# Optimization experiments

Hardware: AMD Instinct MI355X
Metric: run time of the kernel (lower is better)

Reference implementation:

```python
import jax, jax.numpy as jnp
import numpy as np

B, D, H, K = 32768, 784, 500, 50


def setup_inputs() -> dict:
    key = jax.random.key(0)
    ks = jax.random.split(key, 12)
    s = 0.02  # weight init scale
    return {
        "x": jax.random.uniform(ks[0], (B, D), dtype=jnp.float32),
        "u": jax.random.uniform(ks[1], (B, K), dtype=jnp.float32),
        "enc_w1": jax.random.normal(ks[2], (D, H), dtype=jnp.float32) * s,
        "enc_b1": jnp.zeros((H,), jnp.float32),
        "w_alpha": jax.random.normal(ks[3], (H, K), dtype=jnp.float32) * s,
        "b_alpha": jnp.zeros((K,), jnp.float32),
        "w_beta": jax.random.normal(ks[4], (H, K), dtype=jnp.float32) * s,
        "b_beta": jnp.zeros((K,), jnp.float32),
        "dec_w1": jax.random.normal(ks[5], (K, H), dtype=jnp.float32) * s,
        "dec_b1": jnp.zeros((H,), jnp.float32),
        "dec_w2": jax.random.normal(ks[6], (H, D), dtype=jnp.float32) * s,
        "dec_b2": jnp.zeros((D,), jnp.float32),
    }


def reference(x, u, enc_w1, enc_b1, w_alpha, b_alpha, w_beta, b_beta,
              dec_w1, dec_b1, dec_w2, dec_b2):
    # encode
    h = jax.nn.relu(x @ enc_w1 + enc_b1)                       # [B,H]
    alpha = jax.nn.softplus(h @ w_alpha + b_alpha)             # [B,K] > 0
    beta = jax.nn.softplus(h @ w_beta + b_beta)                # [B,K] > 0
    # Kumaraswamy inverse-CDF sample: v = (1 - u^(1/beta))^(1/alpha)
    v = (1.0 - u ** (1.0 / beta)) ** (1.0 / alpha)             # [B,K]
    # stick-breaking: pi[k] = v[k] * prod_{j<k}(1 - v[j])  (exclusive cumprod)
    cp = jnp.cumprod(1.0 - v, axis=-1)                         # [B,K]
    pi = v * jnp.concatenate([jnp.ones_like(v[:, :1]), cp[:, :-1]], axis=-1)
    # decode
    hd = jax.nn.relu(pi @ dec_w1 + dec_b1)                     # [B,H]
    recon_x = jax.nn.sigmoid(hd @ dec_w2 + dec_b2)             # [B,D]
    return recon_x, alpha, beta
```

## Files before the change

### kernel.cpp

```cpp
#include <hip/hip_runtime.h>
#include <math.h>


typedef __bf16 bf16x8 __attribute__((ext_vector_type(8)));
typedef float f32x4 __attribute__((ext_vector_type(4)));

#define BATCH 32768
#define BM 128
#define BN 128
#define BK 64

__device__ __forceinline__ unsigned short bf16_bits(float f) {
    __bf16 b = (__bf16)f;
    return __builtin_bit_cast(unsigned short, b);
}

__device__ __forceinline__ void gll16(const unsigned short* src, unsigned short* ldsdst) {
    __builtin_amdgcn_global_load_lds(
        (const __attribute__((address_space(1))) unsigned int*)src,
        (__attribute__((address_space(3))) unsigned int*)ldsdst,
        16, 0, 0);
}

template<int MODE, bool AF32>
__global__ __launch_bounds__(256) void mfma_gemm(
    const void* __restrict__ Av,
    const unsigned short* __restrict__ Bt,
    const float* __restrict__ bias,
    void* __restrict__ Cv,
    int Kpad, int Kreal, int lda, int ldc, int Nreal, int nbx)
{
    __shared__ unsigned short As[BM * BK];
    __shared__ unsigned short Bs[BN * BK];

    const int nwg = gridDim.x;
    const int orig = blockIdx.x;
    const int q = nwg >> 3, r8 = nwg & 7;
    const int xcd = orig & 7;
    const int chunkbase = (xcd < r8) ? xcd * (q + 1) : r8 * (q + 1) + (xcd - r8) * q;
    const int wgid = chunkbase + (orig >> 3);
    const int bn = wgid % nbx;
    const size_t block_m = (size_t)(wgid / nbx) * BM;
    const int block_n = bn * BN;

    const int tid = threadIdx.x;
    const int l = tid & 63;
    const int wid = tid >> 6;
    const int wr = wid >> 1, wc = wid & 1;

    const int lr = l & 15;
    const int kh = l >> 4;

    f32x4 acc[4][4] = {};

    for (int k0 = 0; k0 < Kpad; k0 += BK) {
        #pragma unroll
        for (int i = 0; i < 4; ++i) {
            int chunk = wid * 4 + i;
            int gid = chunk * 64 + l;
            int r = gid >> 3;
            int kgs = (gid & 7) ^ (r & 7);
            gll16(Bt + (size_t)(block_n + r) * Kpad + k0 + kgs * 8, Bs + chunk * 512);
        }
        if (AF32) {
            const float* Af = (const float*)Av;
            #pragma unroll
            for (int i = 0; i < 4; ++i) {
                int gid = i * 256 + tid;
                int r = gid >> 3, kg = gid & 7;
                int gk = k0 + kg * 8;
                union { __bf16 b[8]; uint4 u4; } pk;
                if (gk < Kreal) {
                    const float4* p = (const float4*)(Af + (block_m + r) * (size_t)lda + gk);
                    float4 f0 = p[0], f1 = p[1];
                    pk.b[0] = (__bf16)f0.x; pk.b[1] = (__bf16)f0.y;
                    pk.b[2] = (__bf16)f0.z; pk.b[3] = (__bf16)f0.w;
                    pk.b[4] = (__bf16)f1.x; pk.b[5] = (__bf16)f1.y;
                    pk.b[6] = (__bf16)f1.z; pk.b[7] = (__bf16)f1.w;
                } else {
                    pk.u4 = make_uint4(0, 0, 0, 0);
                }
                *(uint4*)(As + r * 64 + ((kg ^ (r & 7)) * 8)) = pk.u4;
            }
        } else {
            const unsigned short* Ab = (const unsigned short*)Av;
            #pragma unroll
            for (int i = 0; i < 4; ++i) {
                int chunk = wid * 4 + i;
                int gid = chunk * 64 + l;
                int r = gid >> 3;
                int kgs = (gid & 7) ^ (r & 7);
                gll16(Ab + (block_m + r) * (size_t)lda + k0 + kgs * 8, As + chunk * 512);
            }
        }
        __syncthreads();

        #pragma unroll
        for (int s = 0; s < 2; ++s) {
            bf16x8 af[4], bf[4];
            #pragma unroll
            for (int mi = 0; mi < 4; ++mi) {
                int row = wr * 64 + mi * 16 + lr;
                int g = (s * 4 + kh) ^ (row & 7);
                af[mi] = *(const bf16x8*)(As + row * 64 + g * 8);
            }
            #pragma unroll
            for (int ni = 0; ni < 4; ++ni) {
                int row = wc * 64 + ni * 16 + lr;
                int g = (s * 4 + kh) ^ (row & 7);
                bf[ni] = *(const bf16x8*)(Bs + row * 64 + g * 8);
            }
            #pragma unroll
            for (int mi = 0; mi < 4; ++mi)
                #pragma unroll
                for (int ni = 0; ni < 4; ++ni)
                    acc[mi][ni] = __builtin_amdgcn_mfma_f32_16x16x32_bf16(
                        af[mi], bf[ni], acc[mi][ni], 0, 0, 0);
        }
        __syncthreads();
    }

    const int rg = (l >> 4) * 4;
    #pragma unroll
    for (int mi = 0; mi < 4; ++mi) {
        #pragma unroll
        for (int ni = 0; ni < 4; ++ni) {
            int gn = block_n + wc * 64 + ni * 16 + lr;
            float bs = bias[gn];
            #pragma unroll
            for (int j = 0; j < 4; ++j) {
                long gm = block_m + wr * 64 + mi * 16 + rg + j;
                float z = acc[mi][ni][j] + bs;
                if (MODE == 0) {
                    z = fmaxf(z, 0.f);
                    ((unsigned short*)Cv)[gm * ldc + gn] = bf16_bits(z);
                } else if (MODE == 1) {
                    z = (z > 0.f) ? z + __logf(1.f + __expf(-z))
                                  : __logf(1.f + __expf(z));
                    float* out = (float*)Cv;
                    if (gn < 50)       out[gm * 50 + gn] = z;
                    else if (gn < 100) out[(size_t)BATCH * 50 + gm * 50 + (gn - 50)] = z;
                } else {
                    if (gn < Nreal) {
                        z = __fdividef(1.f, 1.f + __expf(-z));
                        ((float*)Cv)[gm * Nreal + gn] = z;
                    }
                }
            }
        }
    }
}

__global__ __launch_bounds__(256) void prep_bt(
    const float* __restrict__ W, const float* __restrict__ bias,
    unsigned short* __restrict__ Bt, float* __restrict__ bpad,
    int Kr, int Nr, int Kpad, int Npad)
{
    int idx = blockIdx.x * 256 + threadIdx.x;
    if (idx >= Npad * Kpad) return;
    int n = idx / Kpad, k = idx - n * Kpad;
    float v = (n < Nr && k < Kr) ? W[(size_t)k * Nr + n] : 0.f;
    Bt[idx] = bf16_bits(v);
    if (k == 0) bpad[n] = (n < Nr) ? bias[n] : 0.f;
}

__global__ __launch_bounds__(256) void prep_wab(
    const float* __restrict__ Wa, const float* __restrict__ Wb,
    const float* __restrict__ ba, const float* __restrict__ bb,
    unsigned short* __restrict__ Bt, float* __restrict__ bpad)
{
    int idx = blockIdx.x * 256 + threadIdx.x;
    if (idx >= 128 * 512) return;
    int n = idx >> 9, k = idx & 511;
    float v = 0.f;
    if (k < 500) {
        if (n < 50)       v = Wa[(size_t)k * 50 + n];
        else if (n < 100) v = Wb[(size_t)k * 50 + (n - 50)];
    }
    Bt[idx] = bf16_bits(v);
    if (k == 0) bpad[n] = (n < 50) ? ba[n] : ((n < 100) ? bb[n - 50] : 0.f);
}

__global__ __launch_bounds__(256) void sample_pi(
    const float* __restrict__ u, const float* __restrict__ alpha,
    const float* __restrict__ beta, unsigned short* __restrict__ pib)
{
    int row = (blockIdx.x * 256 + threadIdx.x) >> 6;
    int lane = threadIdx.x & 63;
    size_t base = (size_t)row * 50;

    float v = 0.f, w = 1.f;
    if (lane < 50) {
        float a = alpha[base + lane];
        float b = beta[base + lane];
        float uu = u[base + lane];
        float t = exp2f(__fdividef(log2f(uu), b));
        v = exp2f(__fdividef(log2f(1.f - t), a));
        w = 1.f - v;
    }
    float p = w;
    #pragma unroll
    for (int off = 1; off < 64; off <<= 1) {
        float t = __shfl_up(p, off, 64);
        if (lane >= off) p *= t;
    }
    float ex = __shfl_up(p, 1, 64);
    if (lane == 0) ex = 1.f;
    float pi = v * ex;
    pib[(size_t)row * 64 + lane] = (lane < 50) ? bf16_bits(pi) : (unsigned short)0;
}

extern "C" void kernel_launch(void* const* d_in, const int* in_sizes, int n_in,
                              void* d_out, int out_size, void* d_ws, size_t ws_size,
                              hipStream_t stream) {
    const float* x       = (const float*)d_in[0];
    const float* u       = (const float*)d_in[1];
    const float* enc_w1  = (const float*)d_in[2];
    const float* enc_b1  = (const float*)d_in[3];
    const float* w_alpha = (const float*)d_in[4];
    const float* b_alpha = (const float*)d_in[5];
    const float* w_beta  = (const float*)d_in[6];
    const float* b_beta  = (const float*)d_in[7];
    const float* dec_w1  = (const float*)d_in[8];
    const float* dec_b1  = (const float*)d_in[9];
    const float* dec_w2  = (const float*)d_in[10];
    const float* dec_b2  = (const float*)d_in[11];

    const int D = 784;

    float* out   = (float*)d_out;
    float* recon = out;
    float* alpha = out + (size_t)BATCH * D;

    char* ws = (char*)d_ws;
    unsigned short* w1b  = (unsigned short*)(ws);
    unsigned short* wab  = (unsigned short*)(ws + 851968);
    unsigned short* dw1b = (unsigned short*)(ws + 983040);
    unsigned short* dw2b = (unsigned short*)(ws + 1048576);
    float* bias1  = (float*)(ws + 1966080);
    float* biasab = (float*)(ws + 1968128);
    float* biasd1 = (float*)(ws + 1970688);
    float* biasd2 = (float*)(ws + 1972736);
    unsigned short* h    = (unsigned short*)(ws + 2097152);
    unsigned short* pib  = (unsigned short*)(ws + 35651584);
    unsigned short* hdb  = h;

    prep_bt<<<dim3(512 * 832 / 256), 256, 0, stream>>>(
        enc_w1, enc_b1, w1b, bias1, 784, 500, 832, 512);
    prep_wab<<<dim3(256), 256, 0, stream>>>(w_alpha, w_beta, b_alpha, b_beta, wab, biasab);
    prep_bt<<<dim3(512 * 64 / 256), 256, 0, stream>>>(
        dec_w1, dec_b1, dw1b, biasd1, 50, 500, 64, 512);
    prep_bt<<<dim3(896 * 512 / 256), 256, 0, stream>>>(
        dec_w2, dec_b2, dw2b, biasd2, 500, 784, 512, 896);

    mfma_gemm<0, true><<<dim3((512 / BN) * (BATCH / BM)), 256, 0, stream>>>(
        x, w1b, bias1, h, 832, 784, 784, 512, 500, 512 / BN);

    mfma_gemm<1, false><<<dim3(BATCH / BM), 256, 0, stream>>>(
        h, wab, biasab, alpha, 512, 512, 512, 0, 100, 1);

    sample_pi<<<dim3(BATCH * 64 / 256), 256, 0, stream>>>(
        u, alpha, alpha + (size_t)BATCH * 50, pib);

    mfma_gemm<0, false><<<dim3((512 / BN) * (BATCH / BM)), 256, 0, stream>>>(
        pib, dw1b, biasd1, hdb, 64, 64, 64, 512, 500, 512 / BN);

    mfma_gemm<2, false><<<dim3((896 / BN) * (BATCH / BM)), 256, 0, stream>>>(
        hdb, dw2b, biasd2, recon, 512, 512, 512, 784, 784, 896 / BN);
}
```

Measured before the change: 174.2 us.

## Prefetch next fp32 A tile into registers to overlap loads with MFMA

In the fp32-A GEMM path, global loads for the next K tile of A are now issued into registers before computing the current tile. The loaded values are converted to bf16 and written to LDS in the following iteration, with an explicit vmcnt wait that lets the prefetch stay in flight during the MFMAs. Out-of-range addresses are clamped so loads stay unconditional. This hides global load latency for the first layer (x @ enc_w1) at the cost of extra registers, which may reduce occupancy.

```diff
diff --git a/kernel.cpp b/kernel.cpp
--- a/kernel.cpp
+++ b/kernel.cpp
@@ -53,7 +53,7 @@
 
     f32x4 acc[4][4] = {};
 
-    for (int k0 = 0; k0 < Kpad; k0 += BK) {
+    auto issueB = [&](int k0) {
         #pragma unroll
         for (int i = 0; i < 4; ++i) {
             int chunk = wid * 4 + i;
@@ -62,17 +62,60 @@
             int kgs = (gid & 7) ^ (r & 7);
             gll16(Bt + (size_t)(block_n + r) * Kpad + k0 + kgs * 8, Bs + chunk * 512);
         }
-        if (AF32) {
-            const float* Af = (const float*)Av;
+    };
+
+    auto compute = [&]() {
+        #pragma unroll
+        for (int s = 0; s < 2; ++s) {
+            bf16x8 af[4], bf[4];
+            #pragma unroll
+            for (int mi = 0; mi < 4; ++mi) {
+                int row = wr * 64 + mi * 16 + lr;
+                int g = (s * 4 + kh) ^ (row & 7);
+                af[mi] = *(const bf16x8*)(As + row * 64 + g * 8);
+            }
+            #pragma unroll
+            for (int ni = 0; ni < 4; ++ni) {
+                int row = wc * 64 + ni * 16 + lr;
+                int g = (s * 4 + kh) ^ (row & 7);
+                bf[ni] = *(const bf16x8*)(Bs + row * 64 + g * 8);
+            }
+            #pragma unroll
+            for (int mi = 0; mi < 4; ++mi)
+                #pragma unroll
+                for (int ni = 0; ni < 4; ++ni)
+                    acc[mi][ni] = __builtin_amdgcn_mfma_f32_16x16x32_bf16(
+                        af[mi], bf[ni], acc[mi][ni], 0, 0, 0);
+        }
+    };
+
+    if constexpr (AF32) {
+        const float* Af = (const float*)Av;
+        float4 areg[8];
+        bool aok[4];
+        const int clampk = Kreal - 8;
+
+        auto issueA = [&](int k0) {
             #pragma unroll
             for (int i = 0; i < 4; ++i) {
                 int gid = i * 256 + tid;
                 int r = gid >> 3, kg = gid & 7;
                 int gk = k0 + kg * 8;
+                int gkc = (gk <= clampk) ? gk : clampk;
+                const float4* p = (const float4*)(Af + (block_m + r) * (size_t)lda + gkc);
+                areg[2 * i]     = p[0];
+                areg[2 * i + 1] = p[1];
+                aok[i] = (gk < Kreal);
+            }
+        };
+        auto writeA = [&]() {
+            #pragma unroll
+            for (int i = 0; i < 4; ++i) {
+                int gid = i * 256 + tid;
+                int r = gid >> 3, kg = gid & 7;
                 union { __bf16 b[8]; uint4 u4; } pk;
-                if (gk < Kreal) {
-                    const float4* p = (const float4*)(Af + (block_m + r) * (size_t)lda + gk);
-                    float4 f0 = p[0], f1 = p[1];
+                float4 f0 = areg[2 * i], f1 = areg[2 * i + 1];
+                if (aok[i]) {
                     pk.b[0] = (__bf16)f0.x; pk.b[1] = (__bf16)f0.y;
                     pk.b[2] = (__bf16)f0.z; pk.b[3] = (__bf16)f0.w;
                     pk.b[4] = (__bf16)f1.x; pk.b[5] = (__bf16)f1.y;
@@ -82,8 +125,30 @@
                 }
                 *(uint4*)(As + r * 64 + ((kg ^ (r & 7)) * 8)) = pk.u4;
             }
-        } else {
-            const unsigned short* Ab = (const unsigned short*)Av;
+        };
+
+        const int nt = Kpad / BK;
+        issueA(0);
+        for (int t = 0; t < nt - 1; ++t) {
+            issueB(t * BK);
+            writeA();
+            issueA((t + 1) * BK);
+            asm volatile("s_waitcnt vmcnt(8) lgkmcnt(0)" ::: "memory");
+            __builtin_amdgcn_sched_barrier(0);
+            __builtin_amdgcn_s_barrier();
+            compute();
+            __builtin_amdgcn_s_barrier();
+        }
+        issueB((nt - 1) * BK);
+        writeA();
+        asm volatile("s_waitcnt vmcnt(0) lgkmcnt(0)" ::: "memory");
+        __builtin_amdgcn_sched_barrier(0);
+        __builtin_amdgcn_s_barrier();
+        compute();
+    } else {
+        const unsigned short* Ab = (const unsigned short*)Av;
+        for (int k0 = 0; k0 < Kpad; k0 += BK) {
+            issueB(k0);
             #pragma unroll
             for (int i = 0; i < 4; ++i) {
                 int chunk = wid * 4 + i;
@@ -92,32 +157,10 @@
                 int kgs = (gid & 7) ^ (r & 7);
                 gll16(Ab + (block_m + r) * (size_t)lda + k0 + kgs * 8, As + chunk * 512);
             }
-        }
-        __syncthreads();
-
-        #pragma unroll
-        for (int s = 0; s < 2; ++s) {
-            bf16x8 af[4], bf[4];
-            #pragma unroll
-            for (int mi = 0; mi < 4; ++mi) {
-                int row = wr * 64 + mi * 16 + lr;
-                int g = (s * 4 + kh) ^ (row & 7);
-                af[mi] = *(const bf16x8*)(As + row * 64 + g * 8);
-            }
-            #pragma unroll
-            for (int ni = 0; ni < 4; ++ni) {
-                int row = wc * 64 + ni * 16 + lr;
-                int g = (s * 4 + kh) ^ (row & 7);
-                bf[ni] = *(const bf16x8*)(Bs + row * 64 + g * 8);
-            }
-            #pragma unroll
-            for (int mi = 0; mi < 4; ++mi)
-                #pragma unroll
-                for (int ni = 0; ni < 4; ++ni)
-                    acc[mi][ni] = __builtin_amdgcn_mfma_f32_16x16x32_bf16(
-                        af[mi], bf[ni], acc[mi][ni], 0, 0, 0);
-        }
-        __syncthreads();
+            __syncthreads();
+            compute();
+            __syncthreads();
+        }
     }
 
     const int rg = (l >> 4) * 4;
```

New measurement: 161.8 us. 1.08x faster.
